# Kernel optimization log

Measured on AMD Instinct MI355X. Metric: run time of the kernel, lower is better.

Reference implementation:

```python
import jax, jax.numpy as jnp
import numpy as np

VOCAB = 5000; EMB = 300; AUDIO = 74; HID = 128
D1 = 16; D2 = 16; DIM = D1 * D2
UNITS = 128; CELL = 64; OUT = 1
B = 32; S = 32
NGRAMS = (1, 3)


def _lstm(x, w_ih, w_hh, b_ih, b_hh):
    # PyTorch LSTMCell semantics, gate order i, f, g, o
    Bb = x.shape[0]; H = w_hh.shape[1]
    def step(carry, xt):
        h, c = carry
        gates = xt @ w_ih.T + h @ w_hh.T + b_ih + b_hh
        i, f, g, o = jnp.split(gates, 4, axis=-1)
        c = jax.nn.sigmoid(f) * c + jax.nn.sigmoid(i) * jnp.tanh(g)
        h = jax.nn.sigmoid(o) * jnp.tanh(c)
        return (h, c), h
    init = (jnp.zeros((Bb, H), x.dtype), jnp.zeros((Bb, H), x.dtype))
    _, hs = jax.lax.scan(step, init, jnp.swapaxes(x, 0, 1))
    return jnp.swapaxes(hs, 0, 1)  # (B, S, H)


def _windows(x, n):
    # zero-padded n-gram windows: (B, S, d) -> (B, S, n, d)
    xp = jnp.pad(x, ((0, 0), (0, n - 1), (0, 0)))
    s = x.shape[1]
    return jnp.stack([xp[:, k:k + s, :] for k in range(n)], axis=2)


def setup_inputs() -> dict:
    key = jax.random.key(0)
    ks = jax.random.split(key, 26)
    g = lambda i, shape, sc=0.05: jax.random.normal(ks[i], shape, dtype=jnp.float32) * sc
    return dict(
        word_indexes=jax.random.randint(ks[0], (B, S), 0, VOCAB),
        audio=jax.random.normal(ks[1], (B, S, AUDIO), dtype=jnp.float32),
        lookup_table=g(2, (VOCAB, EMB), 0.5),
        phase_tab0=g(3, (VOCAB, D1), 3.14),
        phase_tab1=g(4, (VOCAB, D2), 3.14),
        w_ih=g(5, (4 * HID, EMB)), w_hh=g(6, (4 * HID, HID)),
        b_ih=g(7, (4 * HID,)), b_hh=g(8, (4 * HID,)),
        w_lin=g(9, (D1, HID)), b_lin=g(10, (D1,)),
        w1=g(11, (D2, AUDIO)), b1=g(12, (D2,)),
        w2=g(13, (D2, D2)), b2=g(14, (D2,)),
        w3=g(15, (D2, D2)), b3=g(16, (D2,)),
        modality_weights=jnp.zeros((2,), jnp.float32),
        meas_r=g(17, (UNITS, DIM), 0.5), meas_i=g(18, (UNITS, DIM), 0.5),
        fw1=g(19, (CELL, UNITS)), fb1=g(20, (CELL,)),
        fw2=g(21, (CELL, CELL)), fb2=g(22, (CELL,)),
        fw3=g(23, (OUT, CELL)), fb3=jnp.zeros((OUT,), jnp.float32),
    )


def reference(word_indexes, audio, lookup_table, phase_tab0, phase_tab1,
              w_ih, w_hh, b_ih, b_hh, w_lin, b_lin,
              w1, b1, w2, b2, w3, b3,
              modality_weights, meas_r, meas_i,
              fw1, fb1, fw2, fb2, fw3, fb3):
    eps = 1e-10
    # amplitude subnets (dropout rates are 0 / eval mode)
    text = lookup_table[word_indexes]                      # (B,S,EMB)
    h = _lstm(text, w_ih, w_hh, b_ih, b_hh)
    amp0 = h @ w_lin.T + b_lin                             # (B,S,D1)
    a = jax.nn.relu(audio @ w1.T + b1)
    a = jax.nn.relu(a @ w2.T + b2)
    amp1 = jax.nn.relu(a @ w3.T + b3)                      # (B,S,D2)
    ph0 = phase_tab0[word_indexes]
    ph1 = phase_tab1[word_indexes]

    def branch(amp, ph):
        norm = jnp.linalg.norm(amp, axis=-1, keepdims=True)
        ampn = amp / (norm + eps)
        return norm, ampn * jnp.cos(ph), ampn * jnp.sin(ph)

    n0, r0, i0 = branch(amp0, ph0)
    n1, r1, i1 = branch(amp1, ph1)
    mw = jax.nn.softmax(modality_weights)
    weight = mw[0] * n0 + mw[1] * n1                       # (B,S,1)

    # sequential complex tensor product across modalities,
    # starting from (real=1, imag=1) as in the original code
    tpr = r0 - i0
    tpi = r0 + i0
    real = jnp.einsum('bsi,bsj->bsij', tpr, r1) - jnp.einsum('bsi,bsj->bsij', tpi, i1)
    imag = jnp.einsum('bsi,bsj->bsij', tpr, i1) + jnp.einsum('bsi,bsj->bsij', tpi, r1)
    real = real.reshape(B, S, DIM)
    imag = imag.reshape(B, S, DIM)

    # measurement kernel: unit-norm complex vectors
    kn = jnp.sqrt(jnp.sum(meas_r ** 2 + meas_i ** 2, axis=-1, keepdims=True)) + eps
    vr = meas_r / kn
    vi = meas_i / kn

    probs = []
    for n in NGRAMS:
        wr = _windows(real, n)                             # (B,S,n,DIM)
        wi = _windows(imag, n)
        ww = jax.nn.softmax(_windows(weight, n)[..., 0], axis=-1)  # (B,S,n)
        # complex mixture: rho = sum_n w_n |v_n><v_n|
        rho_r = (jnp.einsum('bsn,bsni,bsnj->bsij', ww, wr, wr)
                 + jnp.einsum('bsn,bsni,bsnj->bsij', ww, wi, wi))
        rho_i = (jnp.einsum('bsn,bsni,bsnj->bsij', ww, wi, wr)
                 - jnp.einsum('bsn,bsni,bsnj->bsij', ww, wr, wi))
        # measurement: Re(v^H rho v) per unit
        m = (jnp.einsum('bsij,ui,uj->bsu', rho_r, vr, vr)
             + jnp.einsum('bsij,ui,uj->bsu', rho_r, vi, vi)
             + jnp.einsum('bsij,ui,uj->bsu', rho_i, vi, vr)
             - jnp.einsum('bsij,ui,uj->bsu', rho_i, vr, vi))
        probs.append(m)
    probs = jnp.concatenate(probs, axis=1)                 # (B, S*len(NGRAMS), UNITS)
    feat = jnp.max(probs, axis=1)                          # 'max' pooling
    y = jax.nn.relu(feat @ fw1.T + fb1)
    y = jax.nn.relu(y @ fw2.T + fb2)
    return y @ fw3.T + fb3                                 # (B, OUT)
```

## Files before the change

### kernel.cpp

```cpp
#include <hip/hip_runtime.h>
#include <math.h>


static constexpr unsigned XW0_OFF  = 0u;
static constexpr unsigned XW1_OFF  = 524288u;
static constexpr unsigned XMAT_OFF = 1179648u;
static constexpr unsigned WT_OFF   = XMAT_OFF + 524288u;
static constexpr unsigned VPP_OFF  = WT_OFF + 1024u;
static constexpr unsigned PP_OFF   = VPP_OFF + 131072u;
static constexpr unsigned PP_HALF  = 262144u;

static constexpr int WLIN = 0;
static constexpr int W1O  = 2048;
static constexpr int W2O  = 3232;
static constexpr int W3O  = 3488;
static constexpr int AUDO = 3744;
static constexpr int BLIN = 6112;
static constexpr int B1O  = 6128;
static constexpr int B2O  = 6144;
static constexpr int B3O  = 6160;

__global__ __launch_bounds__(256) void k1_xw_gemm(
    const int* __restrict__ widx, const float* __restrict__ lut,
    const float* __restrict__ w_ih, const float* __restrict__ b_ih,
    const float* __restrict__ b_hh,
    const float* __restrict__ mr, const float* __restrict__ mi,
    float* __restrict__ ws)
{
  const int bid = blockIdx.x;
  const int t = threadIdx.x;

  if (bid >= 256) {
    const int u = bid - 256;
    float r  = mr[u * 256 + t];
    float ii = mi[u * 256 + t];
    float sq = r * r + ii * ii;
    #pragma unroll
    for (int off = 1; off < 64; off <<= 1) sq += __shfl_xor(sq, off);
    __shared__ float wsum[4];
    if ((t & 63) == 0) wsum[t >> 6] = sq;
    __syncthreads();
    float tot = wsum[0] + wsum[1] + wsum[2] + wsum[3];
    float inv = 1.0f / (sqrtf(tot) + 1e-10f);
    float vr = r * inv, vi = ii * inv;
    float* vpp = ws + VPP_OFF;
    vpp[(2 * u) * 512 + t]           = vr;
    vpp[(2 * u) * 512 + 256 + t]     = vi;
    vpp[(2 * u + 1) * 512 + t]       = -vi;
    vpp[(2 * u + 1) * 512 + 256 + t] = vr;
    return;
  }

  const int rb = bid & 15, cb = (bid >> 4) & 7, kq = bid >> 7;
  const int R = rb * 64, C = cb * 64;
  const int kbase_g = kq * 152;
  const int ktot = kq ? 148 : 152;

  __shared__ alignas(16) float As[32][68];
  __shared__ alignas(16) float Ws[32][68];

  float acc[4][4] = {};
  const int r0 = (t & 15) * 4, j0 = (t >> 4) * 4;

  for (int kt = 0; kt < 5; ++kt) {
    int kl = ktot - kt * 32; if (kl > 32) kl = 32;
    #pragma unroll
    for (int pass = 0; pass < 2; ++pass) {
      int rr = (t >> 3) + pass * 32;
      int kk4 = (t & 7) * 4;
      float4 av = make_float4(0.f, 0.f, 0.f, 0.f);
      float4 wv = make_float4(0.f, 0.f, 0.f, 0.f);
      if (kk4 < kl) {
        int gk = kbase_g + kt * 32 + kk4;
        int word = widx[R + rr];
        av = *(const float4*)&lut[word * 300 + gk];
        wv = *(const float4*)&w_ih[(C + rr) * 300 + gk];
      }
      As[kk4 + 0][rr] = av.x; As[kk4 + 1][rr] = av.y;
      As[kk4 + 2][rr] = av.z; As[kk4 + 3][rr] = av.w;
      Ws[kk4 + 0][rr] = wv.x; Ws[kk4 + 1][rr] = wv.y;
      Ws[kk4 + 2][rr] = wv.z; Ws[kk4 + 3][rr] = wv.w;
    }
    __syncthreads();
    #pragma unroll
    for (int k = 0; k < 32; ++k) {
      float4 a4 = *(const float4*)&As[k][r0];
      float4 w4 = *(const float4*)&Ws[k][j0];
      float ar[4] = {a4.x, a4.y, a4.z, a4.w};
      float wr[4] = {w4.x, w4.y, w4.z, w4.w};
      #pragma unroll
      for (int i2 = 0; i2 < 4; ++i2)
        #pragma unroll
        for (int j2 = 0; j2 < 4; ++j2)
          acc[i2][j2] = fmaf(ar[i2], wr[j2], acc[i2][j2]);
    }
    __syncthreads();
  }

  float* xw = ws + (kq ? XW1_OFF : XW0_OFF);
  #pragma unroll
  for (int i2 = 0; i2 < 4; ++i2) {
    int row = R + r0 + i2, col = C + j0;
    float4 v = make_float4(acc[i2][0], acc[i2][1], acc[i2][2], acc[i2][3]);
    if (kq == 0) {
      v.x += b_ih[col + 0] + b_hh[col + 0];
      v.y += b_ih[col + 1] + b_hh[col + 1];
      v.z += b_ih[col + 2] + b_hh[col + 2];
      v.w += b_ih[col + 3] + b_hh[col + 3];
    }
    *(float4*)&xw[row * 512 + col] = v;
  }
}

__global__ __launch_bounds__(512, 2) void k2_lstm_mix(
    const float* __restrict__ w_hh, const int* __restrict__ widx,
    const float* __restrict__ audio,
    const float* __restrict__ ph0t, const float* __restrict__ ph1t,
    const float* __restrict__ w_lin, const float* __restrict__ b_lin,
    const float* __restrict__ w1, const float* __restrict__ b1,
    const float* __restrict__ w2, const float* __restrict__ b2,
    const float* __restrict__ w3, const float* __restrict__ b3,
    const float* __restrict__ modw, float* __restrict__ ws)
{
  const int b = blockIdx.x;
  const int t = threadIdx.x;
  const int wv = t >> 6;
  const int l  = t & 63;

  __shared__ alignas(16) float part[2][8][512];
  __shared__ alignas(16) float hist[33][132];
  __shared__ float stage[6176];
  __shared__ float amp0s[32][17], a1s[32][17], a2s[32][17], amp1s[32][17];
  __shared__ float tprs[32][17], tpis[32][17], r1ss[32][17], i1ss[32][17];
  __shared__ float nrm0[32], nrm1[32];

  const float* xw0 = ws + XW0_OFF;
  const float* xw1 = ws + XW1_OFF;

  float4 wA[4][4], wB[4][4];
  #pragma unroll
  for (int g = 0; g < 4; ++g) {
    const float* pA = w_hh + (g * 128 + l) * 128 + wv * 16;
    const float* pB = w_hh + (g * 128 + 64 + l) * 128 + wv * 16;
    #pragma unroll
    for (int c = 0; c < 4; ++c) {
      wA[g][c] = *(const float4*)&pA[c * 4];
      wB[g][c] = *(const float4*)&pB[c * 4];
    }
  }

  const int ju = wv * 16 + (l & 15);
  float c = 0.f;
  float x0 = 0.f, x1 = 0.f, x2 = 0.f, x3 = 0.f;
  if (l < 16) {
    const int base = (b * 32 + 0) * 512 + ju;
    x0 = xw0[base +   0] + xw1[base +   0];
    x1 = xw0[base + 128] + xw1[base + 128];
    x2 = xw0[base + 256] + xw1[base + 256];
    x3 = xw0[base + 384] + xw1[base + 384];
  }
  if (t < 128) hist[0][t] = 0.f;
  __syncthreads();

  {
    const float* hb = &hist[0][wv * 16];
    float aA0=0.f,aA1=0.f,aA2=0.f,aA3=0.f,aB0=0.f,aB1=0.f,aB2=0.f,aB3=0.f;
    #pragma unroll
    for (int cc = 0; cc < 4; ++cc) {
      float4 h4 = *(const float4*)&hb[cc * 4];
      aA0 = fmaf(wA[0][cc].x, h4.x, fmaf(wA[0][cc].y, h4.y, fmaf(wA[0][cc].z, h4.z, fmaf(wA[0][cc].w, h4.w, aA0))));
      aA1 = fmaf(wA[1][cc].x, h4.x, fmaf(wA[1][cc].y, h4.y, fmaf(wA[1][cc].z, h4.z, fmaf(wA[1][cc].w, h4.w, aA1))));
      aA2 = fmaf(wA[2][cc].x, h4.x, fmaf(wA[2][cc].y, h4.y, fmaf(wA[2][cc].z, h4.z, fmaf(wA[2][cc].w, h4.w, aA2))));
      aA3 = fmaf(wA[3][cc].x, h4.x, fmaf(wA[3][cc].y, h4.y, fmaf(wA[3][cc].z, h4.z, fmaf(wA[3][cc].w, h4.w, aA3))));
      aB0 = fmaf(wB[0][cc].x, h4.x, fmaf(wB[0][cc].y, h4.y, fmaf(wB[0][cc].z, h4.z, fmaf(wB[0][cc].w, h4.w, aB0))));
      aB1 = fmaf(wB[1][cc].x, h4.x, fmaf(wB[1][cc].y, h4.y, fmaf(wB[1][cc].z, h4.z, fmaf(wB[1][cc].w, h4.w, aB1))));
      aB2 = fmaf(wB[2][cc].x, h4.x, fmaf(wB[2][cc].y, h4.y, fmaf(wB[2][cc].z, h4.z, fmaf(wB[2][cc].w, h4.w, aB2))));
      aB3 = fmaf(wB[3][cc].x, h4.x, fmaf(wB[3][cc].y, h4.y, fmaf(wB[3][cc].z, h4.z, fmaf(wB[3][cc].w, h4.w, aB3))));
    }
    *(float4*)&part[0][wv][l * 4]       = make_float4(aA0, aA1, aA2, aA3);
    *(float4*)&part[0][wv][256 + l * 4] = make_float4(aB0, aB1, aB2, aB3);
  }
  __syncthreads();

  for (int s = 0; s < 32; ++s) {
    if (l < 16) {
      float g0 = x0, g1 = x1, g2 = x2, g3 = x3;
      #pragma unroll
      for (int w = 0; w < 8; ++w) {
        float4 p = *(const float4*)&part[s & 1][w][ju * 4];
        g0 += p.x; g1 += p.y; g2 += p.z; g3 += p.w;
      }
      float si = 1.f / (1.f + __expf(-g0));
      float sf = 1.f / (1.f + __expf(-g1));
      float tg = 1.f - 2.f / (1.f + __expf(2.f * g2));
      float so = 1.f / (1.f + __expf(-g3));
      c = sf * c + si * tg;
      float tc = 1.f - 2.f / (1.f + __expf(2.f * c));
      hist[s + 1][ju] = so * tc;
      if (s < 31) {
        const int nb = (b * 32 + s + 1) * 512 + ju;
        x0 = xw0[nb +   0] + xw1[nb +   0];
        x1 = xw0[nb + 128] + xw1[nb + 128];
        x2 = xw0[nb + 256] + xw1[nb + 256];
        x3 = xw0[nb + 384] + xw1[nb + 384];
      }
    }
    if (s < 31) {
      const float* hb = &hist[s + 1][wv * 16];
      float aA0=0.f,aA1=0.f,aA2=0.f,aA3=0.f,aB0=0.f,aB1=0.f,aB2=0.f,aB3=0.f;
      #pragma unroll
      for (int cc = 0; cc < 4; ++cc) {
        float4 h4 = *(const float4*)&hb[cc * 4];
        aA0 = fmaf(wA[0][cc].x, h4.x, fmaf(wA[0][cc].y, h4.y, fmaf(wA[0][cc].z, h4.z, fmaf(wA[0][cc].w, h4.w, aA0))));
        aA1 = fmaf(wA[1][cc].x, h4.x, fmaf(wA[1][cc].y, h4.y, fmaf(wA[1][cc].z, h4.z, fmaf(wA[1][cc].w, h4.w, aA1))));
        aA2 = fmaf(wA[2][cc].x, h4.x, fmaf(wA[2][cc].y, h4.y, fmaf(wA[2][cc].z, h4.z, fmaf(wA[2][cc].w, h4.w, aA2))));
        aA3 = fmaf(wA[3][cc].x, h4.x, fmaf(wA[3][cc].y, h4.y, fmaf(wA[3][cc].z, h4.z, fmaf(wA[3][cc].w, h4.w, aA3))));
        aB0 = fmaf(wB[0][cc].x, h4.x, fmaf(wB[0][cc].y, h4.y, fmaf(wB[0][cc].z, h4.z, fmaf(wB[0][cc].w, h4.w, aB0))));
        aB1 = fmaf(wB[1][cc].x, h4.x, fmaf(wB[1][cc].y, h4.y, fmaf(wB[1][cc].z, h4.z, fmaf(wB[1][cc].w, h4.w, aB1))));
        aB2 = fmaf(wB[2][cc].x, h4.x, fmaf(wB[2][cc].y, h4.y, fmaf(wB[2][cc].z, h4.z, fmaf(wB[2][cc].w, h4.w, aB2))));
        aB3 = fmaf(wB[3][cc].x, h4.x, fmaf(wB[3][cc].y, h4.y, fmaf(wB[3][cc].z, h4.z, fmaf(wB[3][cc].w, h4.w, aB3))));
      }
      *(float4*)&part[(s + 1) & 1][wv][l * 4]       = make_float4(aA0, aA1, aA2, aA3);
      *(float4*)&part[(s + 1) & 1][wv][256 + l * 4] = make_float4(aB0, aB1, aB2, aB3);
    }
    __syncthreads();
  }

  const int word_base = b * 32;
  for (int i = t; i < 1544; i += 512) {
    const float* src;
    if (i < 512)       src = w_lin + i * 4;
    else if (i < 808)  src = w1 + (i - 512) * 4;
    else if (i < 872)  src = w2 + (i - 808) * 4;
    else if (i < 936)  src = w3 + (i - 872) * 4;
    else if (i < 1528) src = audio + word_base * 74 + (i - 936) * 4;
    else {
      int j = i - 1528;
      const float* bsrc = (j < 4) ? b_lin : (j < 8) ? b1 : (j < 12) ? b2 : b3;
      src = bsrc + (j & 3) * 4;
    }
    *(float4*)&stage[i * 4] = *(const float4*)src;
  }
  __syncthreads();

  const int s = t >> 4, d = t & 15;
  {
    float acc = stage[BLIN + d];
    const float* wl = &stage[WLIN + d * 128];
    const float* hh = &hist[s + 1][0];
    for (int u = 0; u < 128; ++u) acc = fmaf(hh[u], wl[u], acc);
    amp0s[s][d] = acc;
    float a = stage[B1O + d];
    const float* au = &stage[AUDO + s * 74];
    const float* w1r = &stage[W1O + d * 74];
    for (int k = 0; k < 74; ++k) a = fmaf(au[k], w1r[k], a);
    a1s[s][d] = fmaxf(a, 0.f);
  }
  __syncthreads();
  {
    float a = stage[B2O + d];
    #pragma unroll
    for (int k = 0; k < 16; ++k) a = fmaf(a1s[s][k], stage[W2O + d * 16 + k], a);
    a2s[s][d] = fmaxf(a, 0.f);
  }
  __syncthreads();
  {
    float a = stage[B3O + d];
    #pragma unroll
    for (int k = 0; k < 16; ++k) a = fmaf(a2s[s][k], stage[W3O + d * 16 + k], a);
    amp1s[s][d] = fmaxf(a, 0.f);
  }
  __syncthreads();
  if (t < 32) {
    float sq = 0.f;
    #pragma unroll
    for (int dd = 0; dd < 16; ++dd) sq += amp0s[t][dd] * amp0s[t][dd];
    nrm0[t] = sqrtf(sq);
  } else if (t >= 64 && t < 96) {
    int ss = t - 64;
    float sq = 0.f;
    #pragma unroll
    for (int dd = 0; dd < 16; ++dd) sq += amp1s[ss][dd] * amp1s[ss][dd];
    nrm1[ss] = sqrtf(sq);
  }
  __syncthreads();
  {
    const int word = widx[word_base + s];
    float k0 = amp0s[s][d] / (nrm0[s] + 1e-10f);
    float ph = ph0t[word * 16 + d];
    float cc = cosf(ph), sn = sinf(ph);
    tprs[s][d] = k0 * (cc - sn);
    tpis[s][d] = k0 * (cc + sn);
    float k1v = amp1s[s][d] / (nrm1[s] + 1e-10f);
    float p1 = ph1t[word * 16 + d];
    r1ss[s][d] = k1v * cosf(p1);
    i1ss[s][d] = k1v * sinf(p1);
    if (d == 0) {
      float e0 = __expf(modw[0]), e1 = __expf(modw[1]);
      float mw0 = e0 / (e0 + e1);
      ws[WT_OFF + word_base + s] = mw0 * nrm0[s] + (1.f - mw0) * nrm1[s];
    }
  }
  __syncthreads();
  {
    float* X = ws + XMAT_OFF;
    const int c2 = t;
    const int half = c2 >> 8;
    const int i2 = (c2 >> 4) & 15, j2 = c2 & 15;
    for (int ss = 0; ss < 32; ++ss) {
      float v;
      if (half == 0) v = tprs[ss][i2] * r1ss[ss][j2] - tpis[ss][i2] * i1ss[ss][j2];
      else           v = tprs[ss][i2] * i1ss[ss][j2] + tpis[ss][i2] * r1ss[ss][j2];
      X[(word_base + ss) * 512 + c2] = v;
    }
  }
}

__global__ __launch_bounds__(256) void k4_meas(float* __restrict__ ws)
{
  const int bid = blockIdx.x, t = threadIdx.x;
  const int rb = bid & 15, cb = (bid >> 4) & 3, kq = bid >> 6;
  const int R = rb * 64, C = cb * 64;
  const float* X = ws + XMAT_OFF;
  const float* V = ws + VPP_OFF;
  __shared__ alignas(16) float Xs[32][68];
  __shared__ alignas(16) float Vs[32][68];
  float acc[4][4] = {};
  const int r0 = (t & 15) * 4, j0 = (t >> 4) * 4;

  for (int kt = 0; kt < 4; ++kt) {
    #pragma unroll
    for (int pass = 0; pass < 2; ++pass) {
      int rr = (t >> 3) + pass * 32;
      int kk4 = (t & 7) * 4;
      int gk = kq * 128 + kt * 32 + kk4;
      float4 xv = *(const float4*)&X[(R + rr) * 512 + gk];
      float4 vv = *(const float4*)&V[(C + rr) * 512 + gk];
      Xs[kk4 + 0][rr] = xv.x; Xs[kk4 + 1][rr] = xv.y;
      Xs[kk4 + 2][rr] = xv.z; Xs[kk4 + 3][rr] = xv.w;
      Vs[kk4 + 0][rr] = vv.x; Vs[kk4 + 1][rr] = vv.y;
      Vs[kk4 + 2][rr] = vv.z; Vs[kk4 + 3][rr] = vv.w;
    }
    __syncthreads();
    #pragma unroll
    for (int k = 0; k < 32; ++k) {
      float4 a4 = *(const float4*)&Xs[k][r0];
      float4 w4 = *(const float4*)&Vs[k][j0];
      float ar[4] = {a4.x, a4.y, a4.z, a4.w};
      float wr[4] = {w4.x, w4.y, w4.z, w4.w};
      #pragma unroll
      for (int i2 = 0; i2 < 4; ++i2)
        #pragma unroll
        for (int j2 = 0; j2 < 4; ++j2)
          acc[i2][j2] = fmaf(ar[i2], wr[j2], acc[i2][j2]);
    }
    __syncthreads();
  }
  float* Pp = ws + PP_OFF + (unsigned)kq * PP_HALF;
  #pragma unroll
  for (int i2 = 0; i2 < 4; ++i2) {
    float4 v = make_float4(acc[i2][0], acc[i2][1], acc[i2][2], acc[i2][3]);
    *(float4*)&Pp[(R + r0 + i2) * 256 + C + j0] = v;
  }
}

__global__ __launch_bounds__(512) void k5_final(
    const float* __restrict__ fw1, const float* __restrict__ fb1,
    const float* __restrict__ fw2, const float* __restrict__ fb2,
    const float* __restrict__ fw3, const float* __restrict__ fb3,
    const float* __restrict__ ws, float* __restrict__ out)
{
  const int b = blockIdx.x, t = threadIdx.x;
  const int u = t & 127, sg = t >> 7;
  __shared__ float ewt[34];
  __shared__ float pl[32][128];
  __shared__ float fred[4][128];
  __shared__ float feat[128], y1[64], y2[64];
  if (t < 32) ewt[t] = __expf(ws[WT_OFF + b * 32 + t]);
  if (t >= 32 && t < 34) ewt[t] = 1.f;
  __syncthreads();

  const float* Pp = ws + PP_OFF;
  #pragma unroll
  for (int i = 0; i < 8; ++i) {
    int s = sg * 8 + i;
    int bs = b * 32 + s;
    float A = 0.f, Bv = 0.f;
    #pragma unroll
    for (int kq = 0; kq < 4; ++kq) {
      A  += Pp[kq * PP_HALF + bs * 256 + 2 * u];
      Bv += Pp[kq * PP_HALF + bs * 256 + 2 * u + 1];
    }
    pl[s][u] = A * A + Bv * Bv;
  }
  __syncthreads();

  float m = -1e30f;
  #pragma unroll
  for (int i = 0; i < 8; ++i) {
    int s = sg * 8 + i;
    float p0 = pl[s][u];
    m = fmaxf(m, p0);
    float e0 = ewt[s], e1 = ewt[s + 1], e2 = ewt[s + 2];
    float num = e0 * p0;
    if (s + 1 < 32) num += e1 * pl[s + 1][u];
    if (s + 2 < 32) num += e2 * pl[s + 2][u];
    m = fmaxf(m, num / (e0 + e1 + e2));
  }
  fred[sg][u] = m;
  __syncthreads();
  if (t < 128)
    feat[t] = fmaxf(fmaxf(fred[0][t], fred[1][t]), fmaxf(fred[2][t], fred[3][t]));
  __syncthreads();
  if (t < 64) {
    float acc = fb1[t];
    for (int k = 0; k < 128; ++k) acc = fmaf(feat[k], fw1[t * 128 + k], acc);
    y1[t] = fmaxf(acc, 0.f);
  }
  __syncthreads();
  if (t < 64) {
    float acc = fb2[t];
    #pragma unroll
    for (int k = 0; k < 64; ++k) acc = fmaf(y1[k], fw2[t * 64 + k], acc);
    y2[t] = fmaxf(acc, 0.f);
  }
  __syncthreads();
  if (t == 0) {
    float acc = fb3[0];
    #pragma unroll
    for (int k = 0; k < 64; ++k) acc = fmaf(y2[k], fw3[k], acc);
    out[b] = acc;
  }
}

extern "C" void kernel_launch(void* const* d_in, const int* in_sizes, int n_in,
                              void* d_out, int out_size, void* d_ws, size_t ws_size,
                              hipStream_t stream) {
  const int*   widx  = (const int*)d_in[0];
  const float* audio = (const float*)d_in[1];
  const float* lut   = (const float*)d_in[2];
  const float* ph0   = (const float*)d_in[3];
  const float* ph1   = (const float*)d_in[4];
  const float* w_ih  = (const float*)d_in[5];
  const float* w_hh  = (const float*)d_in[6];
  const float* b_ih  = (const float*)d_in[7];
  const float* b_hh  = (const float*)d_in[8];
  const float* w_lin = (const float*)d_in[9];
  const float* b_lin = (const float*)d_in[10];
  const float* w1    = (const float*)d_in[11];
  const float* b1    = (const float*)d_in[12];
  const float* w2    = (const float*)d_in[13];
  const float* b2    = (const float*)d_in[14];
  const float* w3    = (const float*)d_in[15];
  const float* b3    = (const float*)d_in[16];
  const float* modw  = (const float*)d_in[17];
  const float* mr    = (const float*)d_in[18];
  const float* mi    = (const float*)d_in[19];
  const float* fw1   = (const float*)d_in[20];
  const float* fb1   = (const float*)d_in[21];
  const float* fw2   = (const float*)d_in[22];
  const float* fb2   = (const float*)d_in[23];
  const float* fw3   = (const float*)d_in[24];
  const float* fb3   = (const float*)d_in[25];
  float* ws  = (float*)d_ws;
  float* out = (float*)d_out;

  k1_xw_gemm<<<dim3(384), dim3(256), 0, stream>>>(widx, lut, w_ih, b_ih, b_hh, mr, mi, ws);
  k2_lstm_mix<<<dim3(32), dim3(512), 0, stream>>>(w_hh, widx, audio, ph0, ph1,
                                                  w_lin, b_lin, w1, b1, w2, b2,
                                                  w3, b3, modw, ws);
  k4_meas<<<dim3(256), dim3(256), 0, stream>>>(ws);
  k5_final<<<dim3(32), dim3(512), 0, stream>>>(fw1, fb1, fw2, fb2, fw3, fb3, ws, out);
}
```

Baseline: 192.7 us.

## Broadcast LSTM hidden state via readlane and prefetch next-step gate inputs

In the LSTM recurrence, each wave now takes the 16 new hidden values it needs straight from registers with readlane, instead of reading them back from the shared hist buffer. The next step's xw loads are issued before the gate math so their latency overlaps it, and the all-zero first step is replaced by zero-filling the partial-sum buffer. w_lin is staged transposed and padded in shared memory to avoid bank conflicts in the projection, and the launch bound minimum blocks drops from 2 to 1. Each lane holds the h value for unit wv*16+l, so the readlane values match the hist slice the old code read. The risk is extra register pressure and different occupancy from the launch-bound change.

```diff
diff --git a/kernel.cpp b/kernel.cpp
--- a/kernel.cpp
+++ b/kernel.cpp
@@ -10,15 +10,18 @@
 static constexpr unsigned PP_OFF   = VPP_OFF + 131072u;
 static constexpr unsigned PP_HALF  = 262144u;
 
-static constexpr int WLIN = 0;
-static constexpr int W1O  = 2048;
-static constexpr int W2O  = 3232;
-static constexpr int W3O  = 3488;
-static constexpr int AUDO = 3744;
-static constexpr int BLIN = 6112;
-static constexpr int B1O  = 6128;
-static constexpr int B2O  = 6144;
-static constexpr int B3O  = 6160;
+static constexpr int W1O  = 0;
+static constexpr int W2O  = 1184;
+static constexpr int W3O  = 1440;
+static constexpr int AUDO = 1696;
+static constexpr int BLIN = 4064;
+static constexpr int B1O  = 4080;
+static constexpr int B2O  = 4096;
+static constexpr int B3O  = 4112;
+
+__device__ __forceinline__ float readl(float v, int lane) {
+  return __uint_as_float(__builtin_amdgcn_readlane(__float_as_uint(v), lane));
+}
 
 __global__ __launch_bounds__(256) void k1_xw_gemm(
     const int* __restrict__ widx, const float* __restrict__ lut,
@@ -112,7 +115,7 @@
   }
 }
 
-__global__ __launch_bounds__(512, 2) void k2_lstm_mix(
+__global__ __launch_bounds__(512, 1) void k2_lstm_mix(
     const float* __restrict__ w_hh, const int* __restrict__ widx,
     const float* __restrict__ audio,
     const float* __restrict__ ph0t, const float* __restrict__ ph1t,
@@ -128,8 +131,9 @@
   const int l  = t & 63;
 
   __shared__ alignas(16) float part[2][8][512];
-  __shared__ alignas(16) float hist[33][132];
-  __shared__ float stage[6176];
+  __shared__ alignas(16) float hist[32][132];
+  __shared__ float wlT[2176];
+  __shared__ float stage[4128];
   __shared__ float amp0s[32][17], a1s[32][17], a2s[32][17], amp1s[32][17];
   __shared__ float tprs[32][17], tpis[32][17], r1ss[32][17], i1ss[32][17];
   __shared__ float nrm0[32], nrm1[32];
@@ -159,31 +163,21 @@
     x2 = xw0[base + 256] + xw1[base + 256];
     x3 = xw0[base + 384] + xw1[base + 384];
   }
-  if (t < 128) hist[0][t] = 0.f;
-  __syncthreads();
-
-  {
-    const float* hb = &hist[0][wv * 16];
-    float aA0=0.f,aA1=0.f,aA2=0.f,aA3=0.f,aB0=0.f,aB1=0.f,aB2=0.f,aB3=0.f;
-    #pragma unroll
-    for (int cc = 0; cc < 4; ++cc) {
-      float4 h4 = *(const float4*)&hb[cc * 4];
-      aA0 = fmaf(wA[0][cc].x, h4.x, fmaf(wA[0][cc].y, h4.y, fmaf(wA[0][cc].z, h4.z, fmaf(wA[0][cc].w, h4.w, aA0))));
-      aA1 = fmaf(wA[1][cc].x, h4.x, fmaf(wA[1][cc].y, h4.y, fmaf(wA[1][cc].z, h4.z, fmaf(wA[1][cc].w, h4.w, aA1))));
-      aA2 = fmaf(wA[2][cc].x, h4.x, fmaf(wA[2][cc].y, h4.y, fmaf(wA[2][cc].z, h4.z, fmaf(wA[2][cc].w, h4.w, aA2))));
-      aA3 = fmaf(wA[3][cc].x, h4.x, fmaf(wA[3][cc].y, h4.y, fmaf(wA[3][cc].z, h4.z, fmaf(wA[3][cc].w, h4.w, aA3))));
-      aB0 = fmaf(wB[0][cc].x, h4.x, fmaf(wB[0][cc].y, h4.y, fmaf(wB[0][cc].z, h4.z, fmaf(wB[0][cc].w, h4.w, aB0))));
-      aB1 = fmaf(wB[1][cc].x, h4.x, fmaf(wB[1][cc].y, h4.y, fmaf(wB[1][cc].z, h4.z, fmaf(wB[1][cc].w, h4.w, aB1))));
-      aB2 = fmaf(wB[2][cc].x, h4.x, fmaf(wB[2][cc].y, h4.y, fmaf(wB[2][cc].z, h4.z, fmaf(wB[2][cc].w, h4.w, aB2))));
-      aB3 = fmaf(wB[3][cc].x, h4.x, fmaf(wB[3][cc].y, h4.y, fmaf(wB[3][cc].z, h4.z, fmaf(wB[3][cc].w, h4.w, aB3))));
-    }
-    *(float4*)&part[0][wv][l * 4]       = make_float4(aA0, aA1, aA2, aA3);
-    *(float4*)&part[0][wv][256 + l * 4] = make_float4(aB0, aB1, aB2, aB3);
-  }
+  *(float4*)&part[0][wv][l * 4]       = make_float4(0.f, 0.f, 0.f, 0.f);
+  *(float4*)&part[0][wv][256 + l * 4] = make_float4(0.f, 0.f, 0.f, 0.f);
   __syncthreads();
 
   for (int s = 0; s < 32; ++s) {
+    float hn = 0.f;
     if (l < 16) {
+      float n0 = 0.f, n1 = 0.f, n2 = 0.f, n3 = 0.f;
+      if (s < 31) {
+        const int nb = (b * 32 + s + 1) * 512 + ju;
+        n0 = xw0[nb +   0]; n1 = xw0[nb + 128];
+        n2 = xw0[nb + 256]; n3 = xw0[nb + 384];
+        n0 += xw1[nb +   0]; n1 += xw1[nb + 128];
+        n2 += xw1[nb + 256]; n3 += xw1[nb + 384];
+      }
       float g0 = x0, g1 = x1, g2 = x2, g3 = x3;
       #pragma unroll
       for (int w = 0; w < 8; ++w) {
@@ -196,29 +190,28 @@
       float so = 1.f / (1.f + __expf(-g3));
       c = sf * c + si * tg;
       float tc = 1.f - 2.f / (1.f + __expf(2.f * c));
-      hist[s + 1][ju] = so * tc;
-      if (s < 31) {
-        const int nb = (b * 32 + s + 1) * 512 + ju;
-        x0 = xw0[nb +   0] + xw1[nb +   0];
-        x1 = xw0[nb + 128] + xw1[nb + 128];
-        x2 = xw0[nb + 256] + xw1[nb + 256];
-        x3 = xw0[nb + 384] + xw1[nb + 384];
-      }
+      hn = so * tc;
+      hist[s][ju] = hn;
+      x0 = n0; x1 = n1; x2 = n2; x3 = n3;
     }
     if (s < 31) {
-      const float* hb = &hist[s + 1][wv * 16];
+      float h00 = readl(hn,  0), h01 = readl(hn,  1), h02 = readl(hn,  2), h03 = readl(hn,  3);
+      float h04 = readl(hn,  4), h05 = readl(hn,  5), h06 = readl(hn,  6), h07 = readl(hn,  7);
+      float h08 = readl(hn,  8), h09 = readl(hn,  9), h10 = readl(hn, 10), h11 = readl(hn, 11);
+      float h12 = readl(hn, 12), h13 = readl(hn, 13), h14 = readl(hn, 14), h15 = readl(hn, 15);
+      float hv[4][4] = {{h00,h01,h02,h03},{h04,h05,h06,h07},
+                        {h08,h09,h10,h11},{h12,h13,h14,h15}};
       float aA0=0.f,aA1=0.f,aA2=0.f,aA3=0.f,aB0=0.f,aB1=0.f,aB2=0.f,aB3=0.f;
       #pragma unroll
       for (int cc = 0; cc < 4; ++cc) {
-        float4 h4 = *(const float4*)&hb[cc * 4];
-        aA0 = fmaf(wA[0][cc].x, h4.x, fmaf(wA[0][cc].y, h4.y, fmaf(wA[0][cc].z, h4.z, fmaf(wA[0][cc].w, h4.w, aA0))));
-        aA1 = fmaf(wA[1][cc].x, h4.x, fmaf(wA[1][cc].y, h4.y, fmaf(wA[1][cc].z, h4.z, fmaf(wA[1][cc].w, h4.w, aA1))));
-        aA2 = fmaf(wA[2][cc].x, h4.x, fmaf(wA[2][cc].y, h4.y, fmaf(wA[2][cc].z, h4.z, fmaf(wA[2][cc].w, h4.w, aA2))));
-        aA3 = fmaf(wA[3][cc].x, h4.x, fmaf(wA[3][cc].y, h4.y, fmaf(wA[3][cc].z, h4.z, fmaf(wA[3][cc].w, h4.w, aA3))));
-        aB0 = fmaf(wB[0][cc].x, h4.x, fmaf(wB[0][cc].y, h4.y, fmaf(wB[0][cc].z, h4.z, fmaf(wB[0][cc].w, h4.w, aB0))));
-        aB1 = fmaf(wB[1][cc].x, h4.x, fmaf(wB[1][cc].y, h4.y, fmaf(wB[1][cc].z, h4.z, fmaf(wB[1][cc].w, h4.w, aB1))));
-        aB2 = fmaf(wB[2][cc].x, h4.x, fmaf(wB[2][cc].y, h4.y, fmaf(wB[2][cc].z, h4.z, fmaf(wB[2][cc].w, h4.w, aB2))));
-        aB3 = fmaf(wB[3][cc].x, h4.x, fmaf(wB[3][cc].y, h4.y, fmaf(wB[3][cc].z, h4.z, fmaf(wB[3][cc].w, h4.w, aB3))));
+        aA0 = fmaf(wA[0][cc].x, hv[cc][0], fmaf(wA[0][cc].y, hv[cc][1], fmaf(wA[0][cc].z, hv[cc][2], fmaf(wA[0][cc].w, hv[cc][3], aA0))));
+        aA1 = fmaf(wA[1][cc].x, hv[cc][0], fmaf(wA[1][cc].y, hv[cc][1], fmaf(wA[1][cc].z, hv[cc][2], fmaf(wA[1][cc].w, hv[cc][3], aA1))));
+        aA2 = fmaf(wA[2][cc].x, hv[cc][0], fmaf(wA[2][cc].y, hv[cc][1], fmaf(wA[2][cc].z, hv[cc][2], fmaf(wA[2][cc].w, hv[cc][3], aA2))));
+        aA3 = fmaf(wA[3][cc].x, hv[cc][0], fmaf(wA[3][cc].y, hv[cc][1], fmaf(wA[3][cc].z, hv[cc][2], fmaf(wA[3][cc].w, hv[cc][3], aA3))));
+        aB0 = fmaf(wB[0][cc].x, hv[cc][0], fmaf(wB[0][cc].y, hv[cc][1], fmaf(wB[0][cc].z, hv[cc][2], fmaf(wB[0][cc].w, hv[cc][3], aB0))));
+        aB1 = fmaf(wB[1][cc].x, hv[cc][0], fmaf(wB[1][cc].y, hv[cc][1], fmaf(wB[1][cc].z, hv[cc][2], fmaf(wB[1][cc].w, hv[cc][3], aB1))));
+        aB2 = fmaf(wB[2][cc].x, hv[cc][0], fmaf(wB[2][cc].y, hv[cc][1], fmaf(wB[2][cc].z, hv[cc][2], fmaf(wB[2][cc].w, hv[cc][3], aB2))));
+        aB3 = fmaf(wB[3][cc].x, hv[cc][0], fmaf(wB[3][cc].y, hv[cc][1], fmaf(wB[3][cc].z, hv[cc][2], fmaf(wB[3][cc].w, hv[cc][3], aB3))));
       }
       *(float4*)&part[(s + 1) & 1][wv][l * 4]       = make_float4(aA0, aA1, aA2, aA3);
       *(float4*)&part[(s + 1) & 1][wv][256 + l * 4] = make_float4(aB0, aB1, aB2, aB3);
@@ -227,15 +220,22 @@
   }
 
   const int word_base = b * 32;
-  for (int i = t; i < 1544; i += 512) {
+  {
+    const int d = t >> 5, u0 = (t & 31) * 4;
+    float4 v = *(const float4*)&w_lin[d * 128 + u0];
+    wlT[(u0 + 0) * 17 + d] = v.x;
+    wlT[(u0 + 1) * 17 + d] = v.y;
+    wlT[(u0 + 2) * 17 + d] = v.z;
+    wlT[(u0 + 3) * 17 + d] = v.w;
+  }
+  for (int i = t; i < 1032; i += 512) {
     const float* src;
-    if (i < 512)       src = w_lin + i * 4;
-    else if (i < 808)  src = w1 + (i - 512) * 4;
-    else if (i < 872)  src = w2 + (i - 808) * 4;
-    else if (i < 936)  src = w3 + (i - 872) * 4;
-    else if (i < 1528) src = audio + word_base * 74 + (i - 936) * 4;
+    if (i < 296)       src = w1 + i * 4;
+    else if (i < 360)  src = w2 + (i - 296) * 4;
+    else if (i < 424)  src = w3 + (i - 360) * 4;
+    else if (i < 1016) src = audio + word_base * 74 + (i - 424) * 4;
     else {
-      int j = i - 1528;
+      int j = i - 1016;
       const float* bsrc = (j < 4) ? b_lin : (j < 8) ? b1 : (j < 12) ? b2 : b3;
       src = bsrc + (j & 3) * 4;
     }
@@ -246,9 +246,8 @@
   const int s = t >> 4, d = t & 15;
   {
     float acc = stage[BLIN + d];
-    const float* wl = &stage[WLIN + d * 128];
-    const float* hh = &hist[s + 1][0];
-    for (int u = 0; u < 128; ++u) acc = fmaf(hh[u], wl[u], acc);
+    const float* hh = &hist[s][0];
+    for (int u = 0; u < 128; ++u) acc = fmaf(hh[u], wlT[u * 17 + d], acc);
     amp0s[s][d] = acc;
     float a = stage[B1O + d];
     const float* au = &stage[AUDO + s * 74];
```

Result: faster. 186.9 us (-3.0%).
